# Kernel tuning notes

Hardware: AMD Instinct MI355X
Metric: run time of the kernel (lower is better)

## Reference

```python
import jax, jax.numpy as jnp
import numpy as np

N_NODES = 100000
N_EDGES = 1600000
C = 64


def _spline_conv(x, src, dst, u, w, root, bias, n_nodes):
    """SplineConv, dim=1, kernel_size=2, degree=1, open spline, aggr='mean'.

    For K=2, degree=1, pseudo u in [0,1]: basis = (1-u) on knot 0, u on knot 1.
    message_e = (1-u_e) * x[src_e] @ w[0] + u_e * x[src_e] @ w[1]
    Compute the two GEMMs at node level (N < E) then gather, which is
    mathematically identical and cheaper.
    """
    h0 = x @ w[0]  # [N, C]
    h1 = x @ w[1]  # [N, C]
    uc = u[:, None]  # [E, 1]
    msg = (1.0 - uc) * h0[src] + uc * h1[src]  # [E, C]
    agg = jax.ops.segment_sum(msg, dst, num_segments=n_nodes)  # [N, C]
    deg = jax.ops.segment_sum(jnp.ones_like(u), dst, num_segments=n_nodes)
    agg = agg / jnp.maximum(deg, 1.0)[:, None]  # mean aggregation
    return agg + x @ root + bias


def setup_inputs() -> dict:
    key = jax.random.key(0)
    ks = jax.random.split(key, 10)
    x = jax.random.normal(ks[0], (N_NODES, C), dtype=jnp.float32)
    edge_index = jax.random.randint(ks[1], (2, N_EDGES), 0, N_NODES, dtype=jnp.int64)
    edge_attr = jax.random.uniform(ks[2], (N_EDGES, 1), dtype=jnp.float32)
    s = 1.0 / np.sqrt(C)
    w1 = jax.random.uniform(ks[3], (2, C, C), jnp.float32, -s, s)
    root1 = jax.random.uniform(ks[4], (C, C), jnp.float32, -s, s)
    b1 = jnp.zeros((C,), jnp.float32)
    w2 = jax.random.uniform(ks[5], (2, C, C), jnp.float32, -s, s)
    root2 = jax.random.uniform(ks[6], (C, C), jnp.float32, -s, s)
    b2 = jnp.zeros((C,), jnp.float32)
    return {"x": x, "edge_index": edge_index, "edge_attr": edge_attr,
            "w1": w1, "root1": root1, "b1": b1,
            "w2": w2, "root2": root2, "b2": b2}


def reference(x, edge_index, edge_attr, w1, root1, b1, w2, root2, b2):
    src, dst = edge_index[0], edge_index[1]
    u = edge_attr[:, 0]
    n = x.shape[0]
    h = _spline_conv(x, src, dst, u, w1, root1, b1, n)
    h = _spline_conv(h, src, dst, u, w2, root2, b2, n)
    return h
```

## Files before the change

kernel.cpp:

```cpp
#include <hip/hip_runtime.h>

#define CDIM 64

typedef __attribute__((ext_vector_type(8))) short bf16x8;
typedef __attribute__((ext_vector_type(4))) float f32x4;

__device__ __forceinline__ short bf16r(float f) {
    unsigned a = __float_as_uint(f);
    a = (a + 0x7fffu + ((a >> 16) & 1u)) >> 16;
    return (short)a;
}
__device__ __forceinline__ unsigned bfpack(float lo, float hi) {
    unsigned a = __float_as_uint(lo);
    a = (a + 0x7fffu + ((a >> 16) & 1u)) >> 16;
    unsigned b = __float_as_uint(hi);
    b = (b + 0x7fffu + ((b >> 16) & 1u)) & 0xffff0000u;
    return a | b;
}

__global__ __launch_bounds__(256) void k_pack(const float* __restrict__ x,
                                              unsigned* __restrict__ xb32, size_t n2) {
    size_t t = (size_t)blockIdx.x * 256 + threadIdx.x;
    size_t stride = (size_t)gridDim.x * 256;
    for (size_t i = t; i < n2; i += stride) {
        float2 v = ((const float2*)x)[i];
        xb32[i] = bfpack(v.x, v.y);
    }
}

#define NPB_SHIFT 9
#define BKN (1 << NPB_SHIFT)
#define BPAD 10240
#define PART_CH 2048
#define RCAP 1536

__global__ __launch_bounds__(256) void k_prep(int* __restrict__ bkt_cursor, int n_buckets,
                                              const float* __restrict__ w1,
                                              const float* __restrict__ root1,
                                              const float* __restrict__ w2,
                                              const float* __restrict__ root2,
                                              short* __restrict__ wtg) {
    int tid = threadIdx.x;
    if (blockIdx.x == 0) {
        if (tid < n_buckets) bkt_cursor[tid] = tid * BPAD;
        return;
    }
    int l = blockIdx.x - 1;
    const float* s0 = l ? w2 : w1;
    const float* srcs[3] = {s0, s0 + 4096, l ? root2 : root1};
    short* o = wtg + (size_t)l * 3 * 4096;
    for (int i = tid; i < 12288; i += 256) {
        int m = i >> 12, r = i & 4095, k = r >> 6, n = r & 63;
        o[(m << 12) + (n << 6) + k] = bf16r(srcs[m][r]);
    }
}

__global__ __launch_bounds__(256) void k_part(const int* __restrict__ src,
                                              const int* __restrict__ dst,
                                              const float* __restrict__ u,
                                              int* __restrict__ bkt_cursor,
                                              unsigned long long* __restrict__ rec,
                                              int n_edges, int n_buckets) {
    __shared__ int cnt_s[256];
    __shared__ int excl_s[256];
    __shared__ int cur_s[256];
    __shared__ int goff_s[256];
    __shared__ int tot_s;
    __shared__ unsigned long long rec_s[PART_CH];
    __shared__ int tgt_s[PART_CH];
    int tid = threadIdx.x;
    cnt_s[tid] = 0;
    __syncthreads();
    int e0 = blockIdx.x * PART_CH + tid * 8;
    int d[8], s[8];
    float uu[8];
    if (e0 + 8 <= n_edges) {
        int4 d0 = *(const int4*)(dst + e0), d1 = *(const int4*)(dst + e0 + 4);
        int4 s0 = *(const int4*)(src + e0), s1 = *(const int4*)(src + e0 + 4);
        float4 u0 = *(const float4*)(u + e0), u1 = *(const float4*)(u + e0 + 4);
        d[0]=d0.x; d[1]=d0.y; d[2]=d0.z; d[3]=d0.w; d[4]=d1.x; d[5]=d1.y; d[6]=d1.z; d[7]=d1.w;
        s[0]=s0.x; s[1]=s0.y; s[2]=s0.z; s[3]=s0.w; s[4]=s1.x; s[5]=s1.y; s[6]=s1.z; s[7]=s1.w;
        uu[0]=u0.x; uu[1]=u0.y; uu[2]=u0.z; uu[3]=u0.w; uu[4]=u1.x; uu[5]=u1.y; uu[6]=u1.z; uu[7]=u1.w;
    } else {
#pragma unroll
        for (int i = 0; i < 8; ++i) {
            int e = e0 + i;
            bool ok = e < n_edges;
            d[i] = ok ? dst[e] : -1;
            s[i] = ok ? src[e] : 0;
            uu[i] = ok ? u[e] : 0.f;
        }
    }
#pragma unroll
    for (int i = 0; i < 8; ++i)
        if (d[i] >= 0) atomicAdd(&cnt_s[d[i] >> NPB_SHIFT], 1);
    __syncthreads();
    int c = cnt_s[tid];
    excl_s[tid] = c;
    __syncthreads();
    for (int off = 1; off < 256; off <<= 1) {
        int t = (tid >= off) ? excl_s[tid - off] : 0;
        __syncthreads();
        excl_s[tid] += t;
        __syncthreads();
    }
    int excl = excl_s[tid] - c;
    if (tid == 255) tot_s = excl_s[255];
    __syncthreads();
    excl_s[tid] = excl;
    cur_s[tid] = excl;
    goff_s[tid] = (tid < n_buckets && c) ? atomicAdd(&bkt_cursor[tid], c) : 0;
    __syncthreads();
#pragma unroll
    for (int i = 0; i < 8; ++i) {
        if (d[i] >= 0) {
            int b = d[i] >> NPB_SHIFT;
            int p = atomicAdd(&cur_s[b], 1);
            unsigned uq = (unsigned)(uu[i] * 32767.0f + 0.5f);
            rec_s[p] = ((unsigned long long)(unsigned)d[i] << 32)
                     | (unsigned long long)(((unsigned)s[i] << 15) | uq);
            tgt_s[p] = goff_s[b] + (p - excl_s[b]);
        }
    }
    __syncthreads();
    int tot = tot_s;
    for (int i = tid; i < tot; i += 256)
        rec[tgt_s[i]] = rec_s[i];
}

__global__ __launch_bounds__(512) void k_fused(
        const unsigned* __restrict__ xb_in,
        const unsigned long long* __restrict__ rec,
        const int* __restrict__ bkt_cursor,
        const short* __restrict__ wb,
        const float* __restrict__ bias,
        float* __restrict__ out,
        unsigned short* __restrict__ xb_out,
        unsigned* __restrict__ em_g,
        unsigned* __restrict__ rowcnt_g,
        int n_nodes, int n_buckets, int build) {
    __shared__ unsigned em_s[RCAP];
    __shared__ unsigned tmp_em[RCAP];
    __shared__ unsigned short tmp_d[RCAP];
    __shared__ int cnt_s[64];
    __shared__ int row_s[64];
    __shared__ int cur_s[64];
    __shared__ int nm_s;
    __shared__ __align__(16) unsigned gl[64][68];
    int tid = threadIdx.x;
    int blk = blockIdx.x;
    int b = (blk & 7) + 8 * (blk >> 6);
    int sub = (blk >> 3) & 7;
    if (b >= n_buckets) return;
    int lo = (b << NPB_SHIFT) + (sub << 6);
    int region = ((b << 3) + sub) * RCAP;
    const float inv15 = 1.0f / 32767.0f;

    if (build) {
        int nrec = bkt_cursor[b] - b * BPAD;
        const unsigned long long* r0 = rec + (size_t)b * BPAD;
        if (tid < 64) cnt_s[tid] = 0;
        if (tid == 0) nm_s = 0;
        __syncthreads();
        for (int i = tid; i < nrec; i += 512) {
            unsigned long long r = r0[i];
            int rel = (int)(r >> 32) - lo;
            if ((unsigned)rel < 64u) {
                int p = atomicAdd(&nm_s, 1);
                if (p < RCAP) {
                    tmp_em[p] = (unsigned)r;
                    tmp_d[p] = (unsigned short)rel;
                    atomicAdd(&cnt_s[rel], 1);
                }
            }
        }
        __syncthreads();
        if (tid < 64) row_s[tid] = cnt_s[tid];
        __syncthreads();
        for (int off = 1; off < 64; off <<= 1) {
            int t = (tid < 64 && tid >= off) ? row_s[tid - off] : 0;
            __syncthreads();
            if (tid < 64) row_s[tid] += t;
            __syncthreads();
        }
        if (tid < 64) {
            row_s[tid] -= cnt_s[tid];
            cur_s[tid] = row_s[tid];
        }
        __syncthreads();
        int nm = min(nm_s, RCAP);
        for (int i = tid; i < nm; i += 512) {
            int rel = tmp_d[i];
            int p = atomicAdd(&cur_s[rel], 1);
            em_s[p] = tmp_em[i];
        }
        __syncthreads();
        if (tid < 64)
            rowcnt_g[((b << 3) + sub) * 64 + tid] =
                (unsigned)row_s[tid] | ((unsigned)cnt_s[tid] << 16);
        for (int i = tid; i < nm; i += 512) em_g[region + i] = em_s[i];
    } else {
        if (tid < 64) {
            unsigned rc = rowcnt_g[((b << 3) + sub) * 64 + tid];
            row_s[tid] = (int)(rc & 0xffffu);
            cnt_s[tid] = (int)(rc >> 16);
        }
        __syncthreads();
    }

    const unsigned* em = build ? (const unsigned*)&em_s[0] : (em_g + region);
    int qid = tid >> 4;
    int ql = tid & 15;
    for (int t = 0; t < 2; ++t) {
        int rel = qid * 2 + t;
        int start = row_s[rel];
        int cnt = cnt_s[rel];
        int end = start + cnt;
        float a0 = 0.f, a1 = 0.f, a2 = 0.f, a3 = 0.f;
        float b0 = 0.f, b1 = 0.f, b2 = 0.f, b3 = 0.f;
        int j = start;
        for (; j + 4 <= end; j += 4) {
            unsigned e[4]; uint2 v[4];
#pragma unroll
            for (int i = 0; i < 4; ++i) e[i] = em[j + i];
#pragma unroll
            for (int i = 0; i < 4; ++i)
                v[i] = *(const uint2*)(xb_in + (size_t)(e[i] >> 15) * 32 + 2 * ql);
#pragma unroll
            for (int i = 0; i < 4; ++i) {
                float uu = (float)(e[i] & 0x7fffu) * inv15;
                float wa = 1.0f - uu;
                float c0 = __uint_as_float(v[i].x << 16);
                float c1 = __uint_as_float(v[i].x & 0xffff0000u);
                float c2 = __uint_as_float(v[i].y << 16);
                float c3 = __uint_as_float(v[i].y & 0xffff0000u);
                a0 += wa * c0; a1 += wa * c1; a2 += wa * c2; a3 += wa * c3;
                b0 += uu * c0; b1 += uu * c1; b2 += uu * c2; b3 += uu * c3;
            }
        }
        if (j < end) {
            unsigned e[4]; uint2 v[4]; float m[4];
#pragma unroll
            for (int i = 0; i < 4; ++i) {
                int idx = j + i;
                bool ok = idx < end;
                e[i] = em[ok ? idx : (end - 1)];
                m[i] = ok ? 1.0f : 0.0f;
            }
#pragma unroll
            for (int i = 0; i < 4; ++i)
                v[i] = *(const uint2*)(xb_in + (size_t)(e[i] >> 15) * 32 + 2 * ql);
#pragma unroll
            for (int i = 0; i < 4; ++i) {
                float uu = (float)(e[i] & 0x7fffu) * inv15;
                float wa = (1.0f - uu) * m[i], wu = uu * m[i];
                float c0 = __uint_as_float(v[i].x << 16);
                float c1 = __uint_as_float(v[i].x & 0xffff0000u);
                float c2 = __uint_as_float(v[i].y << 16);
                float c3 = __uint_as_float(v[i].y & 0xffff0000u);
                a0 += wa * c0; a1 += wa * c1; a2 += wa * c2; a3 += wa * c3;
                b0 += wu * c0; b1 += wu * c1; b2 += wu * c2; b3 += wu * c3;
            }
        }
        float s = 1.0f / fmaxf((float)cnt, 1.0f);
        *(uint2*)&gl[rel][2 * ql] = make_uint2(bfpack(a0 * s, a1 * s), bfpack(a2 * s, a3 * s));
        *(uint2*)&gl[rel][32 + 2 * ql] = make_uint2(bfpack(b0 * s, b1 * s), bfpack(b2 * s, b3 * s));
    }
    __syncthreads();

    int wv = tid >> 6;
    int lane = tid & 63;
    int tile = wv & 3;
    int nthalf = wv >> 2;
    int quad = lane >> 4;
    int m16 = lane & 15;
    int rown = tile * 16 + m16;
    int arow = lo + rown;
    bool rowok = arow < n_nodes;
    const short* gp = (const short*)&gl[rown][0];
    const unsigned* xp = xb_in + (size_t)arow * 32;
    bf16x8 zf = {0, 0, 0, 0, 0, 0, 0, 0};
    bf16x8 aG0[2], aG1[2], aX[2];
#pragma unroll
    for (int kf = 0; kf < 2; ++kf) {
        aG0[kf] = *(const bf16x8*)(gp + kf * 32 + quad * 8);
        aG1[kf] = *(const bf16x8*)(gp + 64 + kf * 32 + quad * 8);
        aX[kf] = rowok ? *(const bf16x8*)(xp + kf * 16 + quad * 4) : zf;
    }
#pragma unroll
    for (int nh = 0; nh < 2; ++nh) {
        int nt = nthalf * 2 + nh;
        f32x4 accv = {0.f, 0.f, 0.f, 0.f};
#pragma unroll
        for (int kf = 0; kf < 2; ++kf) {
            int col = nt * 16 + m16;
            bf16x8 bw0 = *(const bf16x8*)(wb + (col << 6) + kf * 32 + quad * 8);
            bf16x8 bw1 = *(const bf16x8*)(wb + ((64 + col) << 6) + kf * 32 + quad * 8);
            bf16x8 bwR = *(const bf16x8*)(wb + ((128 + col) << 6) + kf * 32 + quad * 8);
            accv = __builtin_amdgcn_mfma_f32_16x16x32_bf16(aG0[kf], bw0, accv, 0, 0, 0);
            accv = __builtin_amdgcn_mfma_f32_16x16x32_bf16(aG1[kf], bw1, accv, 0, 0, 0);
            accv = __builtin_amdgcn_mfma_f32_16x16x32_bf16(aX[kf], bwR, accv, 0, 0, 0);
        }
        float bcol = bias[nt * 16 + m16];
#pragma unroll
        for (int r = 0; r < 4; ++r) {
            int node = lo + tile * 16 + quad * 4 + r;
            if (node < n_nodes) {
                size_t off = (size_t)node * CDIM + nt * 16 + m16;
                float o = accv[r] + bcol;
                if (out) out[off] = o;
                if (xb_out) xb_out[off] = (unsigned short)bf16r(o);
            }
        }
    }
}

extern "C" void kernel_launch(void* const* d_in, const int* in_sizes, int n_in,
                              void* d_out, int out_size, void* d_ws, size_t ws_size,
                              hipStream_t stream) {
    const float* x = (const float*)d_in[0];
    const int* edge_index = (const int*)d_in[1];
    const float* edge_attr = (const float*)d_in[2];
    const float* w1 = (const float*)d_in[3];
    const float* root1 = (const float*)d_in[4];
    const float* b1 = (const float*)d_in[5];
    const float* w2 = (const float*)d_in[6];
    const float* root2 = (const float*)d_in[7];
    const float* b2 = (const float*)d_in[8];

    int n_nodes = in_sizes[0] / CDIM;
    int n_edges = in_sizes[2];
    const int* src = edge_index;
    const int* dst = edge_index + n_edges;

    size_t F = (size_t)n_nodes * CDIM;
    int n_buckets = (n_nodes + BKN - 1) >> NPB_SHIFT;
    int nb8 = n_buckets * 8;
    unsigned* xbA = (unsigned*)d_ws;
    unsigned* xbB = xbA + F / 2;
    int* bkt_cursor = (int*)(xbB + F / 2);
    uintptr_t p = (uintptr_t)(bkt_cursor + n_buckets);
    p = (p + 15) & ~(uintptr_t)15;
    short* wtg = (short*)p;
    p += (size_t)2 * 3 * 4096 * sizeof(short);
    p = (p + 15) & ~(uintptr_t)15;
    unsigned* em_g = (unsigned*)p;
    p += (size_t)nb8 * RCAP * sizeof(unsigned);
    unsigned* rowcnt_g = (unsigned*)p;
    p += (size_t)nb8 * 64 * sizeof(unsigned);
    p = (p + 15) & ~(uintptr_t)15;
    unsigned long long* rec = (unsigned long long*)p;
    float* out = (float*)d_out;

    int gP = (n_edges + PART_CH - 1) / PART_CH;
    int gF = 64 * ((n_buckets + 7) / 8);

    k_pack<<<2048, 256, 0, stream>>>(x, xbA, F / 2);
    k_prep<<<3, 256, 0, stream>>>(bkt_cursor, n_buckets, w1, root1, w2, root2, wtg);
    k_part<<<gP, 256, 0, stream>>>(src, dst, edge_attr, bkt_cursor, rec, n_edges, n_buckets);

    k_fused<<<gF, 512, 0, stream>>>(xbA, rec, bkt_cursor, wtg, b1,
                                    nullptr, (unsigned short*)xbB,
                                    em_g, rowcnt_g, n_nodes, n_buckets, 1);
    k_fused<<<gF, 512, 0, stream>>>(xbB, rec, bkt_cursor, wtg + 3 * 4096, b2,
                                    out, nullptr,
                                    em_g, rowcnt_g, n_nodes, n_buckets, 0);
}
```

Before: 263.0 us.

## Merge pack/prep/partition into one launch and balance rows by edge count

```diff
diff --git a/kernel.cpp b/kernel.cpp
--- a/kernel.cpp
+++ b/kernel.cpp
@@ -18,49 +18,20 @@
     return a | b;
 }
 
-__global__ __launch_bounds__(256) void k_pack(const float* __restrict__ x,
-                                              unsigned* __restrict__ xb32, size_t n2) {
-    size_t t = (size_t)blockIdx.x * 256 + threadIdx.x;
-    size_t stride = (size_t)gridDim.x * 256;
-    for (size_t i = t; i < n2; i += stride) {
-        float2 v = ((const float2*)x)[i];
-        xb32[i] = bfpack(v.x, v.y);
-    }
-}
-
 #define NPB_SHIFT 9
 #define BKN (1 << NPB_SHIFT)
 #define BPAD 10240
 #define PART_CH 2048
 #define RCAP 1536
 
-__global__ __launch_bounds__(256) void k_prep(int* __restrict__ bkt_cursor, int n_buckets,
-                                              const float* __restrict__ w1,
-                                              const float* __restrict__ root1,
-                                              const float* __restrict__ w2,
-                                              const float* __restrict__ root2,
-                                              short* __restrict__ wtg) {
-    int tid = threadIdx.x;
-    if (blockIdx.x == 0) {
-        if (tid < n_buckets) bkt_cursor[tid] = tid * BPAD;
-        return;
-    }
-    int l = blockIdx.x - 1;
-    const float* s0 = l ? w2 : w1;
-    const float* srcs[3] = {s0, s0 + 4096, l ? root2 : root1};
-    short* o = wtg + (size_t)l * 3 * 4096;
-    for (int i = tid; i < 12288; i += 256) {
-        int m = i >> 12, r = i & 4095, k = r >> 6, n = r & 63;
-        o[(m << 12) + (n << 6) + k] = bf16r(srcs[m][r]);
-    }
-}
-
-__global__ __launch_bounds__(256) void k_part(const int* __restrict__ src,
-                                              const int* __restrict__ dst,
-                                              const float* __restrict__ u,
-                                              int* __restrict__ bkt_cursor,
-                                              unsigned long long* __restrict__ rec,
-                                              int n_edges, int n_buckets) {
+__global__ __launch_bounds__(256) void k_build(
+        const int* __restrict__ src, const int* __restrict__ dst,
+        const float* __restrict__ u, int* __restrict__ bkt_cursor,
+        unsigned long long* __restrict__ rec, int n_edges, int n_buckets, int gP,
+        const float* __restrict__ x, unsigned* __restrict__ xb32, size_t n2,
+        const float* __restrict__ w1, const float* __restrict__ root1,
+        const float* __restrict__ w2, const float* __restrict__ root2,
+        short* __restrict__ wtg) {
     __shared__ int cnt_s[256];
     __shared__ int excl_s[256];
     __shared__ int cur_s[256];
@@ -69,9 +40,32 @@
     __shared__ unsigned long long rec_s[PART_CH];
     __shared__ int tgt_s[PART_CH];
     int tid = threadIdx.x;
+    int bid = blockIdx.x;
+
+    if (bid >= gP) {
+        int r = bid - gP;
+        if (r < 2) {
+            const float* s0 = r ? w2 : w1;
+            const float* srcs[3] = {s0, s0 + 4096, r ? root2 : root1};
+            short* o = wtg + (size_t)r * 3 * 4096;
+            for (int i = tid; i < 12288; i += 256) {
+                int m = i >> 12, rr = i & 4095, k = rr >> 6, n = rr & 63;
+                o[(m << 12) + (n << 6) + k] = bf16r(srcs[m][rr]);
+            }
+        } else {
+            size_t t = (size_t)(r - 2) * 256 + tid;
+            size_t stride = (size_t)(gridDim.x - gP - 2) * 256;
+            for (size_t i = t; i < n2; i += stride) {
+                float2 v = ((const float2*)x)[i];
+                xb32[i] = bfpack(v.x, v.y);
+            }
+        }
+        return;
+    }
+
     cnt_s[tid] = 0;
     __syncthreads();
-    int e0 = blockIdx.x * PART_CH + tid * 8;
+    int e0 = bid * PART_CH + tid * 8;
     int d[8], s[8];
     float uu[8];
     if (e0 + 8 <= n_edges) {
@@ -109,7 +103,8 @@
     __syncthreads();
     excl_s[tid] = excl;
     cur_s[tid] = excl;
-    goff_s[tid] = (tid < n_buckets && c) ? atomicAdd(&bkt_cursor[tid], c) : 0;
+    goff_s[tid] = 0;
+    if (tid < n_buckets && c) goff_s[tid] = tid * BPAD + atomicAdd(&bkt_cursor[tid], c);
     __syncthreads();
 #pragma unroll
     for (int i = 0; i < 8; ++i) {
@@ -145,6 +140,7 @@
     __shared__ int cnt_s[64];
     __shared__ int row_s[64];
     __shared__ int cur_s[64];
+    __shared__ unsigned char ord_s[64];
     __shared__ int nm_s;
     __shared__ __align__(16) unsigned gl[64][68];
     int tid = threadIdx.x;
@@ -157,7 +153,7 @@
     const float inv15 = 1.0f / 32767.0f;
 
     if (build) {
-        int nrec = bkt_cursor[b] - b * BPAD;
+        int nrec = bkt_cursor[b];
         const unsigned long long* r0 = rec + (size_t)b * BPAD;
         if (tid < 64) cnt_s[tid] = 0;
         if (tid == 0) nm_s = 0;
@@ -208,11 +204,24 @@
         __syncthreads();
     }
 
+    if (tid < 64) {
+        int cc = cnt_s[tid];
+        int r = 0;
+        for (int j = 0; j < 64; ++j) {
+            int cj = cnt_s[j];
+            r += (cj > cc) || (cj == cc && j < tid);
+        }
+        ord_s[r] = (unsigned char)tid;
+    }
+    __syncthreads();
+
     const unsigned* em = build ? (const unsigned*)&em_s[0] : (em_g + region);
-    int qid = tid >> 4;
+    int wv0 = tid >> 6;
+    int qw = (tid >> 4) & 3;
     int ql = tid & 15;
     for (int t = 0; t < 2; ++t) {
-        int rel = qid * 2 + t;
+        int grank = t ? (15 - wv0) : wv0;
+        int rel = ord_s[4 * grank + qw];
         int start = row_s[rel];
         int cnt = cnt_s[rel];
         int end = start + cnt;
@@ -353,11 +362,13 @@
     float* out = (float*)d_out;
 
     int gP = (n_edges + PART_CH - 1) / PART_CH;
+    int gB = gP + 2 + 2048;
     int gF = 64 * ((n_buckets + 7) / 8);
 
-    k_pack<<<2048, 256, 0, stream>>>(x, xbA, F / 2);
-    k_prep<<<3, 256, 0, stream>>>(bkt_cursor, n_buckets, w1, root1, w2, root2, wtg);
-    k_part<<<gP, 256, 0, stream>>>(src, dst, edge_attr, bkt_cursor, rec, n_edges, n_buckets);
+    hipMemsetAsync(bkt_cursor, 0, n_buckets * sizeof(int), stream);
+    k_build<<<gB, 256, 0, stream>>>(src, dst, edge_attr, bkt_cursor, rec,
+                                    n_edges, n_buckets, gP,
+                                    x, xbA, F / 2, w1, root1, w2, root2, wtg);
 
     k_fused<<<gF, 512, 0, stream>>>(xbA, rec, bkt_cursor, wtg, b1,
                                     nullptr, (unsigned short*)xbB,
```

New measurement: 269.5 us. 2.5% more time.
